# Kernel tuning notes

Hardware: AMD Instinct MI355X
Metric: run time of the kernel (lower is better)

The kernel has to match this reference:

```python
import math
import jax, jax.numpy as jnp
import numpy as np

B, N, L, E, H, T = 64, 8, 128, 768, 12, 64


def setup_inputs() -> dict:
    key = jax.random.key(0)
    ks = jax.random.split(key, 8)
    s = 0.02
    return {
        "x":  jax.random.normal(ks[0], (B, N, L, E), dtype=jnp.float32),
        # torch Linear weights are [out, in]
        "Wq": jax.random.normal(ks[1], (H, E, E), dtype=jnp.float32) * s,
        "bq": jax.random.normal(ks[2], (H, E), dtype=jnp.float32) * s,
        "Wv": jax.random.normal(ks[3], (H, T, E), dtype=jnp.float32) * s,
        "bv": jax.random.normal(ks[4], (H, T), dtype=jnp.float32) * s,
        "Wf": jax.random.normal(ks[5], (E, H * T), dtype=jnp.float32) * s,
        "bf": jax.random.normal(ks[6], (E,), dtype=jnp.float32) * s,
    }


def reference(x, Wq, bq, Wv, bv, Wf, bf):
    b, n, l, e = x.shape
    S = b * n                      # set_size after the view(-1, L, E)
    x2 = x.reshape(S, l, e)
    # per-head query projection (batched over heads)
    Q = jnp.einsum('sle,hfe->hslf', x2, Wq) + bq[:, None, None, :]      # [H,S,L,E]
    # raw (unsoftmaxed) attention: (Q K^T) V / sqrt(E)
    scores = jnp.einsum('hslf,smf->hslm', Q, x2)                        # [H,S,L,L]
    attn = jnp.einsum('hslm,sme->hsle', scores, x2) * (1.0 / math.sqrt(e))
    # per-head value projection to transformer_dim
    V = jnp.einsum('hsle,hte->hslt', attn, Wv) + bv[:, None, None, :]   # [H,S,L,T]
    # concat heads along last dim (head order preserved)
    cat = jnp.transpose(V, (1, 2, 0, 3)).reshape(S, l, -1)              # [S,L,H*T]
    out = cat @ Wf.T + bf                                               # [S,L,E]
    return out.reshape(b, n, l, e)
```

## Files before the change

kernel.cpp:

```cpp
#include <hip/hip_runtime.h>
#include <stdint.h>


#define EE 768

typedef short s16x8 __attribute__((ext_vector_type(8)));
typedef float f32x4 __attribute__((ext_vector_type(4)));

__device__ __forceinline__ short f2bf(float f){
  union { float fv; uint32_t u; } v; v.fv = f;
  uint32_t r = (v.u + 0x7fffu + ((v.u >> 16) & 1u)) >> 16;
  return (short)r;
}

__device__ __forceinline__ void gld_lds16(const short* g, short* l){
  __builtin_amdgcn_global_load_lds(
      (const __attribute__((address_space(1))) void*)(uintptr_t)g,
      (__attribute__((address_space(3))) void*)(uintptr_t)l,
      16, 0, 0);
}

__device__ __forceinline__ int xcd_swz(int bid, int nwg){
  int xcd = bid & 7, loc = bid >> 3;
  int q = nwg >> 3, r = nwg & 7;
  return (xcd < r ? xcd * (q + 1) : r * (q + 1) + (xcd - r) * q) + loc;
}

__device__ __forceinline__ int swz(int row, int colShort){
  return colShort ^ ((row & 7) << 3);
}

__global__ __launch_bounds__(256) void cast_bf16_k(const float* __restrict__ src,
                                                   short* __restrict__ dst,
                                                   long n, float scale){
  long i = ((long)blockIdx.x * 256 + threadIdx.x) * 8;
  if(i >= n) return;
  float4 a = *(const float4*)(src + i);
  float4 b = *(const float4*)(src + i + 4);
  s16x8 o;
  o[0]=f2bf(a.x*scale); o[1]=f2bf(a.y*scale); o[2]=f2bf(a.z*scale); o[3]=f2bf(a.w*scale);
  o[4]=f2bf(b.x*scale); o[5]=f2bf(b.y*scale); o[6]=f2bf(b.z*scale); o[7]=f2bf(b.w*scale);
  *(s16x8*)(dst + i) = o;
}

__global__ __launch_bounds__(256) void cvec_k(const float* __restrict__ Wf,
                                              const float* __restrict__ bv,
                                              const float* __restrict__ bfv,
                                              float* __restrict__ c){
  int e = blockIdx.x * 256 + threadIdx.x;
  if(e >= EE) return;
  float s = bfv[e];
  for(int k = 0; k < EE; ++k) s += Wf[(long)e * EE + k] * bv[k];
  c[e] = s;
}

__global__ __launch_bounds__(256) void bias_build(const float* __restrict__ bq,
                                                  float* __restrict__ biasQP){
  int i = blockIdx.x * 256 + threadIdx.x;
  if(i < 9984) biasQP[i] = (i < 9216) ? bq[i] : 0.f;
}

template<bool OUTF32>
__global__ __launch_bounds__(256, 2) void gemm_bt(const short* __restrict__ A,
                                                  const short* __restrict__ B,
                                                  const float* __restrict__ bias,
                                                  void* __restrict__ Cout,
                                                  int N, int K){
  __shared__ short smem[4 * 8192];
  const int tid = threadIdx.x, lane = tid & 63, w = tid >> 6;
  const int wr = w >> 1, wc = w & 1;
  const int nCol = N >> 7;
  const int xcd = blockIdx.x & 7, loc = blockIdx.x >> 3;
  const int width = nCol << 3;
  const int gid = loc / width, rem = loc % width;
  const int rowBlk = (xcd << 6) + (gid << 3) + (rem & 7);
  const int colBlk = rem >> 3;
  const long rowA0 = (long)rowBlk << 7;
  const long colB0 = (long)colBlk << 7;
  const int lr = lane >> 3;
  const int sA = swz(lr, (lane & 7) * 8);

  f32x4 acc[4][4] = {};
  const int NT = K >> 6;

  auto stage = [&](int b, int kt){
    short* As = smem + b * 16384;
    #pragma unroll
    for(int it = 0; it < 4; ++it){
      int r = it * 32 + w * 8;
      gld_lds16(&A[(rowA0 + r + lr) * K + kt + sA], &As[r * 64]);
      gld_lds16(&B[(colB0 + r + lr) * K + kt + sA], &As[8192 + r * 64]);
    }
  };

  stage(0, 0);
  for(int t = 0; t < NT; ++t){
    const int cur = t & 1;
    if(t + 1 < NT){
      stage(cur ^ 1, (t + 1) * 64);
      asm volatile("s_waitcnt vmcnt(8)\n\ts_barrier" ::: "memory");
    } else {
      asm volatile("s_waitcnt vmcnt(0)\n\ts_barrier" ::: "memory");
    }
    const short* As = smem + cur * 16384;
    const short* Bs = As + 8192;
    #pragma unroll
    for(int kk = 0; kk < 2; ++kk){
      s16x8 af[4], bfr[4];
      #pragma unroll
      for(int m = 0; m < 4; ++m){
        int row = wr * 64 + m * 16 + (lane & 15);
        af[m] = *(const s16x8*)&As[row * 64 + swz(row, kk * 32 + (lane >> 4) * 8)];
      }
      #pragma unroll
      for(int n = 0; n < 4; ++n){
        int row = wc * 64 + n * 16 + (lane & 15);
        bfr[n] = *(const s16x8*)&Bs[row * 64 + swz(row, kk * 32 + (lane >> 4) * 8)];
      }
      #pragma unroll
      for(int m = 0; m < 4; ++m)
        #pragma unroll
        for(int n = 0; n < 4; ++n)
          acc[m][n] = __builtin_amdgcn_mfma_f32_16x16x32_bf16(af[m], bfr[n], acc[m][n], 0, 0, 0);
    }
    asm volatile("s_barrier" ::: "memory");
  }

  if constexpr(!OUTF32){
    short* Cs = smem;
    #pragma unroll
    for(int n = 0; n < 4; ++n){
      const long col = colB0 + wc * 64 + n * 16 + (lane & 15);
      const float bb = bias ? bias[col] : 0.f;
      #pragma unroll
      for(int m = 0; m < 4; ++m)
        #pragma unroll
        for(int r = 0; r < 4; ++r){
          int row = wr * 64 + m * 16 + (lane >> 4) * 4 + r;
          int c = wc * 64 + n * 16 + (lane & 15);
          Cs[row * 128 + (c ^ ((row & 7) * 8))] = f2bf(acc[m][n][r] + bb);
        }
    }
    __syncthreads();
    short* Co = (short*)Cout;
    #pragma unroll
    for(int k2 = 0; k2 < 8; ++k2){
      int row = k2 * 16 + (tid >> 4);
      int cl = (tid & 15) * 8;
      s16x8 v = *(const s16x8*)&Cs[row * 128 + (cl ^ ((row & 7) * 8))];
      *(s16x8*)&Co[(rowA0 + row) * N + colB0 + cl] = v;
    }
  } else {
    float* Co = (float*)Cout;
    const long crow0 = rowA0 + wr * 64;
    const long ccol0 = colB0 + wc * 64;
    #pragma unroll
    for(int n = 0; n < 4; ++n){
      const long col = ccol0 + n * 16 + (lane & 15);
      const float bb = bias ? bias[col] : 0.f;
      #pragma unroll
      for(int m = 0; m < 4; ++m)
        #pragma unroll
        for(int r = 0; r < 4; ++r){
          const long row = crow0 + m * 16 + (lane >> 4) * 4 + r;
          Co[row * N + col] = acc[m][n][r] + bb;
        }
    }
  }
}

__global__ __launch_bounds__(256, 2) void attn_k(const short* __restrict__ Q, int QS,
                                                 const short* __restrict__ P, int PS,
                                                 const short* __restrict__ X,
                                                 short* __restrict__ Cat,
                                                 int h0, int nH){
  __shared__ short smem[4 * 8192];
  const int tid = threadIdx.x, lane = tid & 63, w = tid >> 6;
  const int wr = w >> 1, wc = w & 1;
  const int nwg = nH << 9;
  const int bid = xcd_swz(blockIdx.x, nwg);
  const int s = bid / nH, hi = bid - s * nH, h = h0 + hi;
  const long row0 = (long)s * 128;
  const int lr = lane >> 3;
  const int sA = swz(lr, (lane & 7) * 8);

  const int pm = tid >> 3, pt0 = (tid & 7) * 8;
  s16x8 pv[4];
  #pragma unroll
  for(int i = 0; i < 4; ++i)
    pv[i] = *(const s16x8*)&P[(row0 + pm + i * 32) * (long)PS + h * 64 + pt0];

  f32x4 acc[4][4] = {};
  auto stage = [&](int b, int kt){
    short* As = smem + b * 16384;
    #pragma unroll
    for(int it = 0; it < 4; ++it){
      int r = it * 32 + w * 8;
      gld_lds16(&Q[(row0 + r + lr) * (long)QS + hi * 768 + kt + sA], &As[r * 64]);
      gld_lds16(&X[(row0 + r + lr) * 768L + kt + sA], &As[8192 + r * 64]);
    }
  };

  stage(0, 0);
  for(int t = 0; t < 12; ++t){
    const int cur = t & 1;
    if(t < 11){
      stage(cur ^ 1, (t + 1) * 64);
      asm volatile("s_waitcnt vmcnt(8)\n\ts_barrier" ::: "memory");
    } else {
      asm volatile("s_waitcnt vmcnt(0)\n\ts_barrier" ::: "memory");
    }
    const short* As = smem + cur * 16384;
    const short* Bs = As + 8192;
    #pragma unroll
    for(int kk = 0; kk < 2; ++kk){
      s16x8 af[4], bfr[4];
      #pragma unroll
      for(int m = 0; m < 4; ++m){
        int row = wr * 64 + m * 16 + (lane & 15);
        af[m] = *(const s16x8*)&As[row * 64 + swz(row, kk * 32 + (lane >> 4) * 8)];
      }
      #pragma unroll
      for(int n = 0; n < 4; ++n){
        int row = wc * 64 + n * 16 + (lane & 15);
        bfr[n] = *(const s16x8*)&Bs[row * 64 + swz(row, kk * 32 + (lane >> 4) * 8)];
      }
      #pragma unroll
      for(int m = 0; m < 4; ++m)
        #pragma unroll
        for(int n = 0; n < 4; ++n)
          acc[m][n] = __builtin_amdgcn_mfma_f32_16x16x32_bf16(af[m], bfr[n], acc[m][n], 0, 0, 0);
    }
    asm volatile("s_barrier" ::: "memory");
  }

  short* Pt = smem;
  short* Vt = smem + 8192;
  short* Ss = smem + 16384;

  #pragma unroll
  for(int m = 0; m < 4; ++m)
    #pragma unroll
    for(int n = 0; n < 4; ++n)
      #pragma unroll
      for(int r = 0; r < 4; ++r){
        int row = wr * 64 + m * 16 + (lane >> 4) * 4 + r;
        int c = wc * 64 + n * 16 + (lane & 15);
        Ss[row * 128 + (c ^ ((row & 7) * 8))] = f2bf(acc[m][n][r]);
      }
  #pragma unroll
  for(int i = 0; i < 4; ++i)
    #pragma unroll
    for(int j = 0; j < 8; ++j){
      int trow = pt0 + j;
      int mc = pm + i * 32;
      Pt[trow * 128 + (mc ^ ((trow & 7) * 8))] = pv[i][j];
    }
  __syncthreads();

  f32x4 accv[2][4] = {};
  #pragma unroll
  for(int kk = 0; kk < 4; ++kk){
    s16x8 a2[2], b4[4];
    #pragma unroll
    for(int m = 0; m < 2; ++m){
      int row = w * 32 + m * 16 + (lane & 15);
      a2[m] = *(const s16x8*)&Ss[row * 128 + ((kk * 32 + (lane >> 4) * 8) ^ ((row & 7) * 8))];
    }
    #pragma unroll
    for(int n = 0; n < 4; ++n){
      int trow = n * 16 + (lane & 15);
      b4[n] = *(const s16x8*)&Pt[trow * 128 + ((kk * 32 + (lane >> 4) * 8) ^ ((trow & 7) * 8))];
    }
    #pragma unroll
    for(int m = 0; m < 2; ++m)
      #pragma unroll
      for(int n = 0; n < 4; ++n)
        accv[m][n] = __builtin_amdgcn_mfma_f32_16x16x32_bf16(a2[m], b4[n], accv[m][n], 0, 0, 0);
  }

  #pragma unroll
  for(int m = 0; m < 2; ++m)
    #pragma unroll
    for(int n = 0; n < 4; ++n)
      #pragma unroll
      for(int r = 0; r < 4; ++r){
        int row = w * 32 + m * 16 + (lane >> 4) * 4 + r;
        int c = n * 16 + (lane & 15);
        Vt[row * 64 + (c ^ ((row & 7) * 8))] = f2bf(accv[m][n][r]);
      }
  __syncthreads();
  #pragma unroll
  for(int k2 = 0; k2 < 4; ++k2){
    int row = k2 * 32 + (tid >> 3);
    int cl = (tid & 7) * 8;
    s16x8 v = *(const s16x8*)&Vt[row * 64 + (cl ^ ((row & 7) * 8))];
    *(s16x8*)&Cat[(row0 + row) * 768L + h * 64 + cl] = v;
  }
}

extern "C" void kernel_launch(void* const* d_in, const int* in_sizes, int n_in,
                              void* d_out, int out_size, void* d_ws, size_t ws_size,
                              hipStream_t stream){
  const float* x  = (const float*)d_in[0];
  const float* Wq = (const float*)d_in[1];
  const float* bq = (const float*)d_in[2];
  const float* Wv = (const float*)d_in[3];
  const float* bv = (const float*)d_in[4];
  const float* Wf = (const float*)d_in[5];
  const float* bfv= (const float*)d_in[6];

  const float rsqE = 0.03608439182435161f;
  char* ws = (char*)d_ws;
  const bool big = ws_size >= 1526507520ULL;

  dim3 b256(256);
  if(big){
    short* Xb   = (short*)(ws + 0L);
    short* QP   = (short*)(ws + 100663296L);
    short* Cat  = (short*)(ws + 1409286144L);
    short* Wb   = (short*)(ws + 1509949440L);
    short* Wfb  = (short*)(ws + 1525284864L);
    float* bQP  = (float*)(ws + 1526464512L);
    float* cv   = (float*)(ws + 1526504448L);

    cast_bf16_k<<<24576, b256, 0, stream>>>(x,  Xb, 50331648L, 1.f);
    cast_bf16_k<<<3456,  b256, 0, stream>>>(Wq, Wb, 7077888L, 1.f);
    cast_bf16_k<<<288,   b256, 0, stream>>>(Wv, Wb + 7077888L, 589824L, rsqE);
    cast_bf16_k<<<288,   b256, 0, stream>>>(Wf, Wfb, 589824L, 1.f);
    bias_build<<<39, b256, 0, stream>>>(bq, bQP);
    cvec_k<<<3, b256, 0, stream>>>(Wf, bv, bfv, cv);

    gemm_bt<false><<<dim3(39936), b256, 0, stream>>>(Xb, Wb, bQP, QP, 9984, 768);
    attn_k<<<dim3(6144), b256, 0, stream>>>(QP, 9984, QP + 9216, 9984, Xb, Cat, 0, 12);
    gemm_bt<true><<<dim3(3072), b256, 0, stream>>>(Cat, Wfb, cv, d_out, 768, 768);
  } else {
    short* Xb   = (short*)(ws + 0L);
    short* Pall = (short*)(ws + 100663296L);
    short* Qbuf = (short*)(ws + 201326592L);
    short* Cat  = (short*)(ws + 301989888L);
    short* Wb   = (short*)(ws + 402653184L);
    short* Wfb  = (short*)(ws + 417988608L);
    float* bQP  = (float*)(ws + 419168256L);
    float* cv   = (float*)(ws + 419208192L);

    cast_bf16_k<<<24576, b256, 0, stream>>>(x,  Xb, 50331648L, 1.f);
    cast_bf16_k<<<3456,  b256, 0, stream>>>(Wq, Wb, 7077888L, 1.f);
    cast_bf16_k<<<288,   b256, 0, stream>>>(Wv, Wb + 7077888L, 589824L, rsqE);
    cast_bf16_k<<<288,   b256, 0, stream>>>(Wf, Wfb, 589824L, 1.f);
    bias_build<<<39, b256, 0, stream>>>(bq, bQP);
    cvec_k<<<3, b256, 0, stream>>>(Wf, bv, bfv, cv);

    gemm_bt<false><<<dim3(3072), b256, 0, stream>>>(Xb, Wb + 7077888L, nullptr, Pall, 768, 768);
    for(int h = 0; h < 12; ++h){
      gemm_bt<false><<<dim3(3072), b256, 0, stream>>>(Xb, Wb + (long)h * 589824L,
                                                      bQP + h * 768, Qbuf, 768, 768);
      attn_k<<<dim3(512), b256, 0, stream>>>(Qbuf, 768, Pall, 768, Xb, Cat, h, 1);
    }
    gemm_bt<true><<<dim3(3072), b256, 0, stream>>>(Cat, Wfb, cv, d_out, 768, 768);
  }
}
```

Before: 1.857 ms.

## Use 256x256 8-wave GEMM for Q projections and group heads by workspace size

```diff
diff --git a/kernel.cpp b/kernel.cpp
--- a/kernel.cpp
+++ b/kernel.cpp
@@ -3,6 +3,7 @@
 
 
 #define EE 768
+#define SLOT 50331648L
 
 typedef short s16x8 __attribute__((ext_vector_type(8)));
 typedef float f32x4 __attribute__((ext_vector_type(4)));
@@ -26,9 +27,8 @@
   return (xcd < r ? xcd * (q + 1) : r * (q + 1) + (xcd - r) * q) + loc;
 }
 
-__device__ __forceinline__ int swz(int row, int colShort){
-  return colShort ^ ((row & 7) << 3);
-}
+__device__ __forceinline__ int swz64(int row, int c){ return c ^ ((row & 7) << 3); }
+__device__ __forceinline__ int swz32(int row, int c){ return c ^ (((row >> 1) & 3) << 3); }
 
 __global__ __launch_bounds__(256) void cast_bf16_k(const float* __restrict__ src,
                                                    short* __restrict__ dst,
@@ -60,16 +60,129 @@
   if(i < 9984) biasQP[i] = (i < 9216) ? bq[i] : 0.f;
 }
 
-template<bool OUTF32>
-__global__ __launch_bounds__(256, 2) void gemm_bt(const short* __restrict__ A,
-                                                  const short* __restrict__ B,
+__global__ __launch_bounds__(512, 1) void gemm256(const short* __restrict__ A,
+                                                  const short* __restrict__ W,
                                                   const float* __restrict__ bias,
-                                                  void* __restrict__ Cout,
-                                                  int N, int K){
+                                                  short* __restrict__ OutBase,
+                                                  int hBase, int nSub, int pSub){
+  __shared__ short lds[2][16384];
+  const int tid = threadIdx.x, lane = tid & 63, w = tid >> 6;
+  const int wr = w >> 2, wc = w & 3;
+  const int bid = xcd_swz(blockIdx.x, nSub * 768);
+  const int g = bid / 768, rb = bid - g * 768;
+  const int rowBlk = rb / 3, colBlk = rb - rowBlk * 3;
+  const long rowA0 = (long)rowBlk * 256;
+  const int colB0 = colBlk * 256;
+  const int wh = (g == pSub) ? 12 : hBase + g;
+  const short* Bm = W + (long)wh * 589824L;
+  short* Out = OutBase + (long)g * SLOT;
+
+  const int sr0 = w * 32 + (lane >> 2);
+  const int sr1 = sr0 + 16;
+  const int scol = (lane & 3) * 8;
+  const int sc0 = swz32(sr0, scol);
+  const int sc1 = swz32(sr1, scol);
+  const short* Ar0 = A + (rowA0 + sr0) * 768;
+  const short* Ar1 = A + (rowA0 + sr1) * 768;
+  const short* Br0 = Bm + (long)(colB0 + sr0) * 768;
+  const short* Br1 = Bm + (long)(colB0 + sr1) * 768;
+
+  f32x4 acc[8][4] = {};
+  s16x8 af[4], bf0[2], bf1[2];
+  const int fr = lane & 15, fc = (lane >> 4) * 8;
+
+  auto stage = [&](int b, int kt){
+    short* Al = &lds[b][0];
+    short* Bl = &lds[b][8192];
+    gld_lds16(Ar0 + kt + sc0, Al + (w * 2) * 512);
+    gld_lds16(Ar1 + kt + sc1, Al + (w * 2 + 1) * 512);
+    gld_lds16(Br0 + kt + sc0, Bl + (w * 2) * 512);
+    gld_lds16(Br1 + kt + sc1, Bl + (w * 2 + 1) * 512);
+  };
+
+  stage(0, 0);
+  for(int t = 0; t < 24; ++t){
+    if(t < 23){
+      stage((t + 1) & 1, (t + 1) * 32);
+      asm volatile("s_waitcnt vmcnt(4)\n\ts_barrier" ::: "memory");
+    } else {
+      asm volatile("s_waitcnt vmcnt(0)\n\ts_barrier" ::: "memory");
+    }
+    const short* Al = &lds[t & 1][0];
+    const short* Bl = &lds[t & 1][8192];
+
+    auto loadA = [&](int mh){
+      #pragma unroll
+      for(int m = 0; m < 4; ++m){
+        int row = wr * 128 + (mh * 4 + m) * 16 + fr;
+        af[m] = *(const s16x8*)&Al[row * 32 + swz32(row, fc)];
+      }
+    };
+    auto loadB = [&](int nh, s16x8* bf){
+      #pragma unroll
+      for(int n = 0; n < 2; ++n){
+        int row = wc * 64 + (nh * 2 + n) * 16 + fr;
+        bf[n] = *(const s16x8*)&Bl[row * 32 + swz32(row, fc)];
+      }
+    };
+    auto mm = [&](int mh, int nh, s16x8* bf){
+      __builtin_amdgcn_s_setprio(1);
+      #pragma unroll
+      for(int m = 0; m < 4; ++m)
+        #pragma unroll
+        for(int n = 0; n < 2; ++n)
+          acc[mh * 4 + m][nh * 2 + n] = __builtin_amdgcn_mfma_f32_16x16x32_bf16(
+              af[m], bf[n], acc[mh * 4 + m][nh * 2 + n], 0, 0, 0);
+      __builtin_amdgcn_s_setprio(0);
+    };
+
+    loadA(0); loadB(0, bf0); mm(0, 0, bf0);
+    loadB(1, bf1);           mm(0, 1, bf1);
+    loadA(1);                mm(1, 1, bf1);
+    loadB(0, bf0);           mm(1, 0, bf0);
+    asm volatile("s_barrier" ::: "memory");
+  }
+
+  float bb[4];
+  #pragma unroll
+  for(int n = 0; n < 4; ++n)
+    bb[n] = bias[wh * 768 + colB0 + wc * 64 + n * 16 + fr];
+
+  short* Cs = &lds[0][0];
+  #pragma unroll
+  for(int ch = 0; ch < 2; ++ch){
+    __syncthreads();
+    if(wr == ch){
+      #pragma unroll
+      for(int m = 0; m < 8; ++m)
+        #pragma unroll
+        for(int n = 0; n < 4; ++n)
+          #pragma unroll
+          for(int r2 = 0; r2 < 4; ++r2){
+            int row = m * 16 + (lane >> 4) * 4 + r2;
+            int c = wc * 64 + n * 16 + fr;
+            Cs[row * 256 + (c ^ (((row >> 2) & 3) << 4))] = f2bf(acc[m][n][r2] + bb[n]);
+          }
+    }
+    __syncthreads();
+    #pragma unroll
+    for(int i = 0; i < 8; ++i){
+      int idx = i * 512 + tid;
+      int row = idx >> 5, cl = (idx & 31) * 8;
+      s16x8 v = *(const s16x8*)&Cs[row * 256 + (cl ^ (((row >> 2) & 3) << 4))];
+      *(s16x8*)&Out[(rowA0 + ch * 128 + row) * 768 + colB0 + cl] = v;
+    }
+  }
+}
+
+__global__ __launch_bounds__(256, 2) void gemm_f32(const short* __restrict__ A,
+                                                   const short* __restrict__ B,
+                                                   const float* __restrict__ bias,
+                                                   float* __restrict__ Cout){
   __shared__ short smem[4 * 8192];
   const int tid = threadIdx.x, lane = tid & 63, w = tid >> 6;
   const int wr = w >> 1, wc = w & 1;
-  const int nCol = N >> 7;
+  const int nCol = 6;
   const int xcd = blockIdx.x & 7, loc = blockIdx.x >> 3;
   const int width = nCol << 3;
   const int gid = loc / width, rem = loc % width;
@@ -78,25 +191,23 @@
   const long rowA0 = (long)rowBlk << 7;
   const long colB0 = (long)colBlk << 7;
   const int lr = lane >> 3;
-  const int sA = swz(lr, (lane & 7) * 8);
+  const int sA = swz64(lr, (lane & 7) * 8);
 
   f32x4 acc[4][4] = {};
-  const int NT = K >> 6;
-
   auto stage = [&](int b, int kt){
     short* As = smem + b * 16384;
     #pragma unroll
     for(int it = 0; it < 4; ++it){
       int r = it * 32 + w * 8;
-      gld_lds16(&A[(rowA0 + r + lr) * K + kt + sA], &As[r * 64]);
-      gld_lds16(&B[(colB0 + r + lr) * K + kt + sA], &As[8192 + r * 64]);
+      gld_lds16(&A[(rowA0 + r + lr) * 768 + kt + sA], &As[r * 64]);
+      gld_lds16(&B[(colB0 + r + lr) * 768 + kt + sA], &As[8192 + r * 64]);
     }
   };
 
   stage(0, 0);
-  for(int t = 0; t < NT; ++t){
+  for(int t = 0; t < 12; ++t){
     const int cur = t & 1;
-    if(t + 1 < NT){
+    if(t < 11){
       stage(cur ^ 1, (t + 1) * 64);
       asm volatile("s_waitcnt vmcnt(8)\n\ts_barrier" ::: "memory");
     } else {
@@ -110,12 +221,12 @@
       #pragma unroll
       for(int m = 0; m < 4; ++m){
         int row = wr * 64 + m * 16 + (lane & 15);
-        af[m] = *(const s16x8*)&As[row * 64 + swz(row, kk * 32 + (lane >> 4) * 8)];
+        af[m] = *(const s16x8*)&As[row * 64 + swz64(row, kk * 32 + (lane >> 4) * 8)];
       }
       #pragma unroll
       for(int n = 0; n < 4; ++n){
         int row = wc * 64 + n * 16 + (lane & 15);
-        bfr[n] = *(const s16x8*)&Bs[row * 64 + swz(row, kk * 32 + (lane >> 4) * 8)];
+        bfr[n] = *(const s16x8*)&Bs[row * 64 + swz64(row, kk * 32 + (lane >> 4) * 8)];
       }
       #pragma unroll
       for(int m = 0; m < 4; ++m)
@@ -126,51 +237,24 @@
     asm volatile("s_barrier" ::: "memory");
   }
 
-  if constexpr(!OUTF32){
-    short* Cs = smem;
-    #pragma unroll
-    for(int n = 0; n < 4; ++n){
-      const long col = colB0 + wc * 64 + n * 16 + (lane & 15);
-      const float bb = bias ? bias[col] : 0.f;
-      #pragma unroll
-      for(int m = 0; m < 4; ++m)
-        #pragma unroll
-        for(int r = 0; r < 4; ++r){
-          int row = wr * 64 + m * 16 + (lane >> 4) * 4 + r;
-          int c = wc * 64 + n * 16 + (lane & 15);
-          Cs[row * 128 + (c ^ ((row & 7) * 8))] = f2bf(acc[m][n][r] + bb);
-        }
-    }
-    __syncthreads();
-    short* Co = (short*)Cout;
-    #pragma unroll
-    for(int k2 = 0; k2 < 8; ++k2){
-      int row = k2 * 16 + (tid >> 4);
-      int cl = (tid & 15) * 8;
-      s16x8 v = *(const s16x8*)&Cs[row * 128 + (cl ^ ((row & 7) * 8))];
-      *(s16x8*)&Co[(rowA0 + row) * N + colB0 + cl] = v;
-    }
-  } else {
-    float* Co = (float*)Cout;
-    const long crow0 = rowA0 + wr * 64;
-    const long ccol0 = colB0 + wc * 64;
-    #pragma unroll
-    for(int n = 0; n < 4; ++n){
-      const long col = ccol0 + n * 16 + (lane & 15);
-      const float bb = bias ? bias[col] : 0.f;
-      #pragma unroll
-      for(int m = 0; m < 4; ++m)
-        #pragma unroll
-        for(int r = 0; r < 4; ++r){
-          const long row = crow0 + m * 16 + (lane >> 4) * 4 + r;
-          Co[row * N + col] = acc[m][n][r] + bb;
-        }
-    }
-  }
-}
-
-__global__ __launch_bounds__(256, 2) void attn_k(const short* __restrict__ Q, int QS,
-                                                 const short* __restrict__ P, int PS,
+  const long crow0 = rowA0 + wr * 64;
+  const long ccol0 = colB0 + wc * 64;
+  #pragma unroll
+  for(int n = 0; n < 4; ++n){
+    const long col = ccol0 + n * 16 + (lane & 15);
+    const float bbv = bias[col];
+    #pragma unroll
+    for(int m = 0; m < 4; ++m)
+      #pragma unroll
+      for(int r = 0; r < 4; ++r){
+        const long row = crow0 + m * 16 + (lane >> 4) * 4 + r;
+        Cout[row * 768 + col] = acc[m][n][r] + bbv;
+      }
+  }
+}
+
+__global__ __launch_bounds__(256, 2) void attn_k(const short* __restrict__ Q,
+                                                 const short* __restrict__ P,
                                                  const short* __restrict__ X,
                                                  short* __restrict__ Cat,
                                                  int h0, int nH){
@@ -182,21 +266,22 @@
   const int s = bid / nH, hi = bid - s * nH, h = h0 + hi;
   const long row0 = (long)s * 128;
   const int lr = lane >> 3;
-  const int sA = swz(lr, (lane & 7) * 8);
+  const int sA = swz64(lr, (lane & 7) * 8);
 
   const int pm = tid >> 3, pt0 = (tid & 7) * 8;
   s16x8 pv[4];
   #pragma unroll
   for(int i = 0; i < 4; ++i)
-    pv[i] = *(const s16x8*)&P[(row0 + pm + i * 32) * (long)PS + h * 64 + pt0];
+    pv[i] = *(const s16x8*)&P[(row0 + pm + i * 32) * 768L + h * 64 + pt0];
 
   f32x4 acc[4][4] = {};
+  const short* Qh = Q + (long)hi * SLOT;
   auto stage = [&](int b, int kt){
     short* As = smem + b * 16384;
     #pragma unroll
     for(int it = 0; it < 4; ++it){
       int r = it * 32 + w * 8;
-      gld_lds16(&Q[(row0 + r + lr) * (long)QS + hi * 768 + kt + sA], &As[r * 64]);
+      gld_lds16(&Qh[(row0 + r + lr) * 768L + kt + sA], &As[r * 64]);
       gld_lds16(&X[(row0 + r + lr) * 768L + kt + sA], &As[8192 + r * 64]);
     }
   };
@@ -218,12 +303,12 @@
       #pragma unroll
       for(int m = 0; m < 4; ++m){
         int row = wr * 64 + m * 16 + (lane & 15);
-        af[m] = *(const s16x8*)&As[row * 64 + swz(row, kk * 32 + (lane >> 4) * 8)];
+        af[m] = *(const s16x8*)&As[row * 64 + swz64(row, kk * 32 + (lane >> 4) * 8)];
       }
       #pragma unroll
       for(int n = 0; n < 4; ++n){
         int row = wc * 64 + n * 16 + (lane & 15);
-        bfr[n] = *(const s16x8*)&Bs[row * 64 + swz(row, kk * 32 + (lane >> 4) * 8)];
+        bfr[n] = *(const s16x8*)&Bs[row * 64 + swz64(row, kk * 32 + (lane >> 4) * 8)];
       }
       #pragma unroll
       for(int m = 0; m < 4; ++m)
@@ -246,7 +331,7 @@
       for(int r = 0; r < 4; ++r){
         int row = wr * 64 + m * 16 + (lane >> 4) * 4 + r;
         int c = wc * 64 + n * 16 + (lane & 15);
-        Ss[row * 128 + (c ^ ((row & 7) * 8))] = f2bf(acc[m][n][r]);
+        Ss[row * 128 + swz64(row, c)] = f2bf(acc[m][n][r]);
       }
   #pragma unroll
   for(int i = 0; i < 4; ++i)
@@ -254,7 +339,7 @@
     for(int j = 0; j < 8; ++j){
       int trow = pt0 + j;
       int mc = pm + i * 32;
-      Pt[trow * 128 + (mc ^ ((trow & 7) * 8))] = pv[i][j];
+      Pt[trow * 128 + swz64(trow, mc)] = pv[i][j];
     }
   __syncthreads();
 
@@ -265,12 +350,12 @@
     #pragma unroll
     for(int m = 0; m < 2; ++m){
       int row = w * 32 + m * 16 + (lane & 15);
-      a2[m] = *(const s16x8*)&Ss[row * 128 + ((kk * 32 + (lane >> 4) * 8) ^ ((row & 7) * 8))];
+      a2[m] = *(const s16x8*)&Ss[row * 128 + swz64(row, kk * 32 + (lane >> 4) * 8)];
     }
     #pragma unroll
     for(int n = 0; n < 4; ++n){
       int trow = n * 16 + (lane & 15);
-      b4[n] = *(const s16x8*)&Pt[trow * 128 + ((kk * 32 + (lane >> 4) * 8) ^ ((trow & 7) * 8))];
+      b4[n] = *(const s16x8*)&Pt[trow * 128 + swz64(trow, kk * 32 + (lane >> 4) * 8)];
     }
     #pragma unroll
     for(int m = 0; m < 2; ++m)
@@ -287,14 +372,14 @@
       for(int r = 0; r < 4; ++r){
         int row = w * 32 + m * 16 + (lane >> 4) * 4 + r;
         int c = n * 16 + (lane & 15);
-        Vt[row * 64 + (c ^ ((row & 7) * 8))] = f2bf(accv[m][n][r]);
+        Vt[row * 64 + swz64(row, c)] = f2bf(accv[m][n][r]);
       }
   __syncthreads();
   #pragma unroll
   for(int k2 = 0; k2 < 4; ++k2){
     int row = k2 * 32 + (tid >> 3);
     int cl = (tid & 7) * 8;
-    s16x8 v = *(const s16x8*)&Vt[row * 64 + (cl ^ ((row & 7) * 8))];
+    s16x8 v = *(const s16x8*)&Vt[row * 64 + swz64(row, cl)];
     *(s16x8*)&Cat[(row0 + row) * 768L + h * 64 + cl] = v;
   }
 }
@@ -312,51 +397,36 @@
 
   const float rsqE = 0.03608439182435161f;
   char* ws = (char*)d_ws;
-  const bool big = ws_size >= 1526507520ULL;
-
-  dim3 b256(256);
-  if(big){
-    short* Xb   = (short*)(ws + 0L);
-    short* QP   = (short*)(ws + 100663296L);
-    short* Cat  = (short*)(ws + 1409286144L);
-    short* Wb   = (short*)(ws + 1509949440L);
-    short* Wfb  = (short*)(ws + 1525284864L);
-    float* bQP  = (float*)(ws + 1526464512L);
-    float* cv   = (float*)(ws + 1526504448L);
-
-    cast_bf16_k<<<24576, b256, 0, stream>>>(x,  Xb, 50331648L, 1.f);
-    cast_bf16_k<<<3456,  b256, 0, stream>>>(Wq, Wb, 7077888L, 1.f);
-    cast_bf16_k<<<288,   b256, 0, stream>>>(Wv, Wb + 7077888L, 589824L, rsqE);
-    cast_bf16_k<<<288,   b256, 0, stream>>>(Wf, Wfb, 589824L, 1.f);
-    bias_build<<<39, b256, 0, stream>>>(bq, bQP);
-    cvec_k<<<3, b256, 0, stream>>>(Wf, bv, bfv, cv);
-
-    gemm_bt<false><<<dim3(39936), b256, 0, stream>>>(Xb, Wb, bQP, QP, 9984, 768);
-    attn_k<<<dim3(6144), b256, 0, stream>>>(QP, 9984, QP + 9216, 9984, Xb, Cat, 0, 12);
-    gemm_bt<true><<<dim3(3072), b256, 0, stream>>>(Cat, Wfb, cv, d_out, 768, 768);
-  } else {
-    short* Xb   = (short*)(ws + 0L);
-    short* Pall = (short*)(ws + 100663296L);
-    short* Qbuf = (short*)(ws + 201326592L);
-    short* Cat  = (short*)(ws + 301989888L);
-    short* Wb   = (short*)(ws + 402653184L);
-    short* Wfb  = (short*)(ws + 417988608L);
-    float* bQP  = (float*)(ws + 419168256L);
-    float* cv   = (float*)(ws + 419208192L);
-
-    cast_bf16_k<<<24576, b256, 0, stream>>>(x,  Xb, 50331648L, 1.f);
-    cast_bf16_k<<<3456,  b256, 0, stream>>>(Wq, Wb, 7077888L, 1.f);
-    cast_bf16_k<<<288,   b256, 0, stream>>>(Wv, Wb + 7077888L, 589824L, rsqE);
-    cast_bf16_k<<<288,   b256, 0, stream>>>(Wf, Wfb, 589824L, 1.f);
-    bias_build<<<39, b256, 0, stream>>>(bq, bQP);
-    cvec_k<<<3, b256, 0, stream>>>(Wf, bv, bfv, cv);
-
-    gemm_bt<false><<<dim3(3072), b256, 0, stream>>>(Xb, Wb + 7077888L, nullptr, Pall, 768, 768);
-    for(int h = 0; h < 12; ++h){
-      gemm_bt<false><<<dim3(3072), b256, 0, stream>>>(Xb, Wb + (long)h * 589824L,
-                                                      bQP + h * 768, Qbuf, 768, 768);
-      attn_k<<<dim3(512), b256, 0, stream>>>(Qbuf, 768, Pall, 768, Xb, Cat, h, 1);
-    }
-    gemm_bt<true><<<dim3(3072), b256, 0, stream>>>(Cat, Wfb, cv, d_out, 768, 768);
-  }
-}
+
+  short* Xb  = (short*)(ws);
+  short* Cat = (short*)(ws + 100663296L);
+  short* Wb  = (short*)(ws + 201326592L);
+  short* Wfb = (short*)(ws + 216662016L);
+  float* bQP = (float*)(ws + 217841664L);
+  float* cv  = (float*)(ws + 217881600L);
+  short* QS  = (short*)(ws + 217884672L);
+
+  const size_t QOFF = 217884672ULL;
+  int G = 1;
+  const int cands[5] = {12, 6, 4, 3, 2};
+  for(int i = 0; i < 5; ++i)
+    if(ws_size >= QOFF + (size_t)(cands[i] + 1) * 100663296ULL){ G = cands[i]; break; }
+  short* Pall = QS + (long)G * SLOT;
+
+  dim3 b256(256), b512(512);
+  cast_bf16_k<<<24576, b256, 0, stream>>>(x,  Xb, 50331648L, 1.f);
+  cast_bf16_k<<<3456,  b256, 0, stream>>>(Wq, Wb, 7077888L, 1.f);
+  cast_bf16_k<<<288,   b256, 0, stream>>>(Wv, Wb + 7077888L, 589824L, rsqE);
+  cast_bf16_k<<<288,   b256, 0, stream>>>(Wf, Wfb, 589824L, 1.f);
+  bias_build<<<39, b256, 0, stream>>>(bq, bQP);
+  cvec_k<<<3, b256, 0, stream>>>(Wf, bv, bfv, cv);
+
+  const int nB = 12 / G;
+  for(int b = 0; b < nB; ++b){
+    const int nSub = G + (b == 0 ? 1 : 0);
+    const int pSub = (b == 0) ? G : -1;
+    gemm256<<<dim3(nSub * 768), b512, 0, stream>>>(Xb, Wb, bQP, QS, b * G, nSub, pSub);
+    attn_k<<<dim3(G * 512), b256, 0, stream>>>(QS, Pall, Xb, Cat, b * G, G);
+  }
+  gemm_f32<<<dim3(3072), b256, 0, stream>>>(Cat, Wfb, cv, (float*)d_out);
+}
```

After: 1.740 ms. -6.3%, faster.
